# Optimization experiments

Measured on AMD Instinct MI355X. Metric: run time of the kernel, lower is better.

Reference implementation:

```python
import jax, jax.numpy as jnp
import numpy as np

ATTR_LEN = [2, 4, 4, 8]  # sums to 18 = MLP output dim; prod = 256 cases
USER_EMB_DIM = 256
B = 8192


def build_cases(attr_len):
    # Cartesian product of per-attribute one-hots -> [prod(attr_len), sum(attr_len)]
    out = np.eye(attr_len[0], dtype=np.float32)
    for n in attr_len[1:]:
        m = np.eye(n, dtype=np.float32)
        out = np.concatenate(
            [np.repeat(out, n, axis=0), np.tile(m, (out.shape[0], 1))], axis=1)
    return out


def setup_inputs() -> dict:
    key = jax.random.key(0)
    ks = jax.random.split(key, 8)
    d = USER_EMB_DIM
    x = jax.random.normal(ks[0], (B, d), dtype=jnp.float32)
    y = jax.random.uniform(ks[1], (B, 18), dtype=jnp.float32)
    # nn.Linear-style params (scaled normals)
    W1 = jax.random.normal(ks[2], (d, 50), dtype=jnp.float32) / np.sqrt(d)
    b1 = jnp.zeros((50,), dtype=jnp.float32)
    W2 = jax.random.normal(ks[3], (50, 32), dtype=jnp.float32) / np.sqrt(50.0)
    b2 = jnp.zeros((32,), dtype=jnp.float32)
    W3 = jax.random.normal(ks[4], (32, 18), dtype=jnp.float32) / np.sqrt(32.0)
    b3 = jnp.zeros((18,), dtype=jnp.float32)
    cases = jnp.asarray(build_cases(ATTR_LEN))  # [256, 18]
    return {"x": x, "y": y, "W1": W1, "b1": b1, "W2": W2, "b2": b2,
            "W3": W3, "b3": b3, "cases": cases}


def reference(x, y, W1, b1, W2, b2, W3, b3, cases):
    # MLP: user_emb_dim -> 50 -> 32 -> 18, sigmoid activations on hidden layers
    h = jax.nn.sigmoid(x @ W1 + b1)
    h = jax.nn.sigmoid(h @ W2 + b2)
    W_user = h @ W3 + b3                                  # [B, 18]
    # Partition function over all combinatorial label cases, fused into one
    # GEMM + logsumexp (original loops over cases with exp+accumulate).
    log_denom = jax.nn.logsumexp(W_user @ cases.T, axis=1)  # [B]
    # obj_i = exp(sum_j W_user[i].y[j]) / denom_i ; loss = -sum log obj
    S = jnp.sum(W_user @ y.T, axis=1)                     # [B] (via [B,B] mm, as original)
    loss = -jnp.sum(S - log_denom)
    # 'logit' in the original is W_user detached to numpy; return the array.
    return W_user, loss
```

## Files before the change

### kernel.cpp

```cpp
#include <hip/hip_runtime.h>

#define NB   8192
#define ND   256
#define NH1  50
#define NH2  32
#define NH3  18
#define RPB  16
#define NBLK (NB / RPB)
#define WSS  40


__device__ __forceinline__ float sigmoidf_fast(float v) {
    return 1.0f / (1.0f + __expf(-v));
}

template <int CTRL>
__device__ __forceinline__ float dpp_addf(float v) {
    return v + __int_as_float(__builtin_amdgcn_update_dpp(
        0, __float_as_int(v), CTRL, 0xF, 0xF, true));
}
__device__ __forceinline__ float sum16(float v) {
    v = dpp_addf<0xB1>(v);
    v = dpp_addf<0x4E>(v);
    v = dpp_addf<0x124>(v);
    v = dpp_addf<0x128>(v);
    return v;
}

__device__ __forceinline__ void gload_lds16(const float* g, float* l) {
    __builtin_amdgcn_global_load_lds(
        (const __attribute__((address_space(1))) unsigned int*)g,
        (__attribute__((address_space(3))) unsigned int*)l, 16, 0, 0);
}

__global__ __launch_bounds__(256) void fused_main(
    const float* __restrict__ x, const float* __restrict__ y,
    const float* __restrict__ W1, const float* __restrict__ b1,
    const float* __restrict__ W2, const float* __restrict__ b2,
    const float* __restrict__ W3, const float* __restrict__ b3,
    float* __restrict__ out, float* __restrict__ ws)
{
    __shared__ alignas(16) float w1l[ND * NH1];
    __shared__ alignas(16) float w2l[NH1 * NH2];
    __shared__ alignas(16) float w3l[NH2 * NH3];
    __shared__ alignas(16) float h2l[RPB][NH2 + 2];
    __shared__ alignas(16) float wul[RPB][NH3 + 1];

    const int t    = threadIdx.x;
    const int row  = t >> 4;
    const int ksl  = t & 15;
    const int lane = t & 63;
    const int wave = t >> 6;
    const int grow = blockIdx.x * RPB + row;

    const float* xrow = x + (size_t)grow * ND + 2 * ksl;
    float2 xv[8];
#pragma unroll
    for (int c = 0; c < 8; ++c)
        xv[c] = *reinterpret_cast<const float2*>(xrow + 32 * c);

#pragma unroll
    for (int i = 0; i < 13; ++i) {
        const int c = wave + 4 * i;
        if (c < 50)
            gload_lds16(W1 + c * 256 + lane * 4, w1l + c * 256);
    }
    for (int e = t; e < NH1 * NH2; e += 256) w2l[e] = W2[e];
    for (int e = t; e < NH2 * NH3; e += 256) w3l[e] = W3[e];
    __syncthreads();

    float h1[NH1];
#pragma unroll
    for (int j = 0; j < NH1; ++j) h1[j] = 0.0f;
#pragma unroll
    for (int c = 0; c < 8; ++c) {
        const int kA = 32 * c + 2 * ksl;
        const float* wA = &w1l[kA * NH1];
        const float* wB = wA + NH1;
        const float xa = xv[c].x, xb = xv[c].y;
#pragma unroll
        for (int jj = 0; jj < 25; ++jj) {
            const float2 a = *reinterpret_cast<const float2*>(wA + 2 * jj);
            const float2 b = *reinterpret_cast<const float2*>(wB + 2 * jj);
            h1[2 * jj]     = fmaf(xa, a.x, fmaf(xb, b.x, h1[2 * jj]));
            h1[2 * jj + 1] = fmaf(xa, a.y, fmaf(xb, b.y, h1[2 * jj + 1]));
        }
    }
#pragma unroll
    for (int j = 0; j < NH1; ++j)
        h1[j] = sigmoidf_fast(sum16(h1[j]) + b1[j]);

    {
        const float2 bb = *reinterpret_cast<const float2*>(b2 + 2 * ksl);
        float h2a = bb.x, h2b = bb.y;
#pragma unroll
        for (int j = 0; j < NH1; ++j) {
            const float2 w = *reinterpret_cast<const float2*>(&w2l[j * NH2 + 2 * ksl]);
            h2a = fmaf(h1[j], w.x, h2a);
            h2b = fmaf(h1[j], w.y, h2b);
        }
        h2a = sigmoidf_fast(h2a);
        h2b = sigmoidf_fast(h2b);
        *reinterpret_cast<float2*>(&h2l[row][2 * ksl]) = make_float2(h2a, h2b);
    }

    {
        float a0 = b3[ksl];
        float a1 = (ksl < 2) ? b3[16 + ksl] : 0.0f;
#pragma unroll
        for (int j = 0; j < NH2; ++j) {
            const float h = h2l[row][j];
            a0 = fmaf(h, w3l[j * NH3 + ksl], a0);
            if (ksl < 2) a1 = fmaf(h, w3l[j * NH3 + 16 + ksl], a1);
        }
        wul[row][ksl] = a0;
        out[(size_t)grow * NH3 + ksl] = a0;
        if (ksl < 2) {
            wul[row][16 + ksl] = a1;
            out[(size_t)grow * NH3 + 16 + ksl] = a1;
        }
    }
    __syncthreads();

    if (t < 64) {
        const bool act = t < RPB;
        float wv[NH3], yv[NH3];
        float ld = 0.0f;
        if (act) {
            const float* yrow = y + (size_t)(blockIdx.x * RPB + t) * NH3;
#pragma unroll
            for (int c = 0; c < NH3; ++c) {
                wv[c] = wul[t][c];
                yv[c] = yrow[c];
            }
            float m = fmaxf(wv[0], wv[1]);
            ld += m + __logf(__expf(wv[0] - m) + __expf(wv[1] - m));
            m = fmaxf(fmaxf(wv[2], wv[3]), fmaxf(wv[4], wv[5]));
            ld += m + __logf(__expf(wv[2] - m) + __expf(wv[3] - m) +
                             __expf(wv[4] - m) + __expf(wv[5] - m));
            m = fmaxf(fmaxf(wv[6], wv[7]), fmaxf(wv[8], wv[9]));
            ld += m + __logf(__expf(wv[6] - m) + __expf(wv[7] - m) +
                             __expf(wv[8] - m) + __expf(wv[9] - m));
            m = wv[10];
#pragma unroll
            for (int i = 11; i < NH3; ++i) m = fmaxf(m, wv[i]);
            float s = 0.0f;
#pragma unroll
            for (int i = 10; i < NH3; ++i) s += __expf(wv[i] - m);
            ld += m + __logf(s);
        } else {
#pragma unroll
            for (int c = 0; c < NH3; ++c) { wv[c] = 0.0f; yv[c] = 0.0f; }
        }

        ld = sum16(ld);
#pragma unroll
        for (int c = 0; c < NH3; ++c) {
            wv[c] = sum16(wv[c]);
            yv[c] = sum16(yv[c]);
        }
        if (t == 0) {
            float* slot = ws + (size_t)blockIdx.x * WSS;
#pragma unroll
            for (int c = 0; c < NH3; ++c) {
                slot[c]       = yv[c];
                slot[NH3 + c] = wv[c];
            }
            slot[36] = ld;
        }
    }
}

__global__ __launch_bounds__(256) void finalize_loss(
    const float* __restrict__ ws, float* __restrict__ out)
{
    __shared__ double part[4][37];
    const int t = threadIdx.x;
    const int w = t >> 6, l = t & 63;
    if (l < 37) {
        double a = 0.0;
        for (int b = w * (NBLK / 4); b < (w + 1) * (NBLK / 4); ++b)
            a += (double)ws[(size_t)b * WSS + l];
        part[w][l] = a;
    }
    __syncthreads();
    if (t == 0) {
        double tot[37];
#pragma unroll
        for (int c = 0; c < 37; ++c)
            tot[c] = part[0][c] + part[1][c] + part[2][c] + part[3][c];
        double s = 0.0;
#pragma unroll
        for (int c = 0; c < NH3; ++c)
            s += tot[NH3 + c] * tot[c];
        out[(size_t)NB * NH3] = (float)(-(s - tot[36]));
    }
}

extern "C" void kernel_launch(void* const* d_in, const int* in_sizes, int n_in,
                              void* d_out, int out_size, void* d_ws, size_t ws_size,
                              hipStream_t stream) {
    const float* x  = (const float*)d_in[0];
    const float* y  = (const float*)d_in[1];
    const float* W1 = (const float*)d_in[2];
    const float* b1 = (const float*)d_in[3];
    const float* W2 = (const float*)d_in[4];
    const float* b2 = (const float*)d_in[5];
    const float* W3 = (const float*)d_in[6];
    const float* b3 = (const float*)d_in[7];
    float* out = (float*)d_out;
    float* ws  = (float*)d_ws;

    fused_main<<<dim3(NBLK), dim3(256), 0, stream>>>(x, y, W1, b1, W2, b2, W3, b3, out, ws);
    finalize_loss<<<dim3(1), dim3(256), 0, stream>>>(ws, out);
}
```

Before: 94.73 us.

## Process two rows per thread with 128-thread blocks to reuse W1 LDS loads

Halves the block size to 128 threads and has each thread compute two batch rows (rs and rs+8). Each W1 value read from LDS now feeds FMAs for both rows, and the reads become float4 instead of paired float2. The goal is to cut LDS read traffic per FMA and the per-block cost of staging W1, W2 and W3. In exchange each thread holds twice as many accumulators (100 h1 values), which raises register pressure and may lower occupancy.

```diff
diff --git a/kernel.cpp b/kernel.cpp
--- a/kernel.cpp
+++ b/kernel.cpp
@@ -6,6 +6,7 @@
 #define NH2  32
 #define NH3  18
 #define RPB  16
+#define TPB  128
 #define NBLK (NB / RPB)
 #define WSS  40
 
@@ -33,7 +34,7 @@
         (__attribute__((address_space(3))) unsigned int*)l, 16, 0, 0);
 }
 
-__global__ __launch_bounds__(256) void fused_main(
+__global__ __launch_bounds__(TPB) void fused_main(
     const float* __restrict__ x, const float* __restrict__ y,
     const float* __restrict__ W1, const float* __restrict__ b1,
     const float* __restrict__ W2, const float* __restrict__ b2,
@@ -47,77 +48,106 @@
     __shared__ alignas(16) float wul[RPB][NH3 + 1];
 
     const int t    = threadIdx.x;
-    const int row  = t >> 4;
+    const int rs   = t >> 4;
     const int ksl  = t & 15;
     const int lane = t & 63;
     const int wave = t >> 6;
-    const int grow = blockIdx.x * RPB + row;
-
-    const float* xrow = x + (size_t)grow * ND + 2 * ksl;
-    float2 xv[8];
-#pragma unroll
-    for (int c = 0; c < 8; ++c)
-        xv[c] = *reinterpret_cast<const float2*>(xrow + 32 * c);
-
-#pragma unroll
-    for (int i = 0; i < 13; ++i) {
-        const int c = wave + 4 * i;
-        if (c < 50)
-            gload_lds16(W1 + c * 256 + lane * 4, w1l + c * 256);
-    }
-    for (int e = t; e < NH1 * NH2; e += 256) w2l[e] = W2[e];
-    for (int e = t; e < NH2 * NH3; e += 256) w3l[e] = W3[e];
+    const int g0   = blockIdx.x * RPB + rs;
+    const int g1   = g0 + 8;
+
+    const float* xr0 = x + (size_t)g0 * ND + 2 * ksl;
+    const float* xr1 = x + (size_t)g1 * ND + 2 * ksl;
+    float2 xv0[8], xv1[8];
+#pragma unroll
+    for (int c = 0; c < 8; ++c) {
+        xv0[c] = *reinterpret_cast<const float2*>(xr0 + 32 * c);
+        xv1[c] = *reinterpret_cast<const float2*>(xr1 + 32 * c);
+    }
+
+#pragma unroll
+    for (int i = 0; i < 25; ++i) {
+        const int c = wave + 2 * i;
+        gload_lds16(W1 + c * 256 + lane * 4, w1l + c * 256);
+    }
+    for (int e = t; e < NH1 * NH2; e += TPB) w2l[e] = W2[e];
+    for (int e = t; e < NH2 * NH3; e += TPB) w3l[e] = W3[e];
     __syncthreads();
 
-    float h1[NH1];
-#pragma unroll
-    for (int j = 0; j < NH1; ++j) h1[j] = 0.0f;
+    float h1a[NH1], h1b[NH1];
+#pragma unroll
+    for (int j = 0; j < NH1; ++j) { h1a[j] = 0.0f; h1b[j] = 0.0f; }
 #pragma unroll
     for (int c = 0; c < 8; ++c) {
         const int kA = 32 * c + 2 * ksl;
-        const float* wA = &w1l[kA * NH1];
-        const float* wB = wA + NH1;
-        const float xa = xv[c].x, xb = xv[c].y;
-#pragma unroll
-        for (int jj = 0; jj < 25; ++jj) {
-            const float2 a = *reinterpret_cast<const float2*>(wA + 2 * jj);
-            const float2 b = *reinterpret_cast<const float2*>(wB + 2 * jj);
-            h1[2 * jj]     = fmaf(xa, a.x, fmaf(xb, b.x, h1[2 * jj]));
-            h1[2 * jj + 1] = fmaf(xa, a.y, fmaf(xb, b.y, h1[2 * jj + 1]));
-        }
-    }
-#pragma unroll
-    for (int j = 0; j < NH1; ++j)
-        h1[j] = sigmoidf_fast(sum16(h1[j]) + b1[j]);
+        const float* wp = &w1l[kA * NH1];
+        const float xa0 = xv0[c].x, xb0 = xv0[c].y;
+        const float xa1 = xv1[c].x, xb1 = xv1[c].y;
+#pragma unroll
+        for (int q = 0; q < 25; ++q) {
+            const float4 w = *reinterpret_cast<const float4*>(wp + 4 * q);
+            const float we[4] = {w.x, w.y, w.z, w.w};
+#pragma unroll
+            for (int s = 0; s < 4; ++s) {
+                const int e = 4 * q + s;
+                if (e < NH1) {
+                    h1a[e] = fmaf(xa0, we[s], h1a[e]);
+                    h1b[e] = fmaf(xa1, we[s], h1b[e]);
+                } else {
+                    h1a[e - NH1] = fmaf(xb0, we[s], h1a[e - NH1]);
+                    h1b[e - NH1] = fmaf(xb1, we[s], h1b[e - NH1]);
+                }
+            }
+        }
+    }
+#pragma unroll
+    for (int j = 0; j < NH1; ++j) {
+        h1a[j] = sigmoidf_fast(sum16(h1a[j]) + b1[j]);
+        h1b[j] = sigmoidf_fast(sum16(h1b[j]) + b1[j]);
+    }
 
     {
         const float2 bb = *reinterpret_cast<const float2*>(b2 + 2 * ksl);
-        float h2a = bb.x, h2b = bb.y;
+        float aa0 = bb.x, aa1 = bb.y, ba0 = bb.x, ba1 = bb.y;
 #pragma unroll
         for (int j = 0; j < NH1; ++j) {
             const float2 w = *reinterpret_cast<const float2*>(&w2l[j * NH2 + 2 * ksl]);
-            h2a = fmaf(h1[j], w.x, h2a);
-            h2b = fmaf(h1[j], w.y, h2b);
-        }
-        h2a = sigmoidf_fast(h2a);
-        h2b = sigmoidf_fast(h2b);
-        *reinterpret_cast<float2*>(&h2l[row][2 * ksl]) = make_float2(h2a, h2b);
+            aa0 = fmaf(h1a[j], w.x, aa0);
+            aa1 = fmaf(h1a[j], w.y, aa1);
+            ba0 = fmaf(h1b[j], w.x, ba0);
+            ba1 = fmaf(h1b[j], w.y, ba1);
+        }
+        *reinterpret_cast<float2*>(&h2l[rs][2 * ksl]) =
+            make_float2(sigmoidf_fast(aa0), sigmoidf_fast(aa1));
+        *reinterpret_cast<float2*>(&h2l[rs + 8][2 * ksl]) =
+            make_float2(sigmoidf_fast(ba0), sigmoidf_fast(ba1));
     }
 
     {
-        float a0 = b3[ksl];
-        float a1 = (ksl < 2) ? b3[16 + ksl] : 0.0f;
+        float a0A = b3[ksl], a0B = b3[ksl];
+        float a1A = (ksl < 2) ? b3[16 + ksl] : 0.0f;
+        float a1B = a1A;
 #pragma unroll
         for (int j = 0; j < NH2; ++j) {
-            const float h = h2l[row][j];
-            a0 = fmaf(h, w3l[j * NH3 + ksl], a0);
-            if (ksl < 2) a1 = fmaf(h, w3l[j * NH3 + 16 + ksl], a1);
-        }
-        wul[row][ksl] = a0;
-        out[(size_t)grow * NH3 + ksl] = a0;
+            const float hA = h2l[rs][j];
+            const float hB = h2l[rs + 8][j];
+            const float w3v = w3l[j * NH3 + ksl];
+            a0A = fmaf(hA, w3v, a0A);
+            a0B = fmaf(hB, w3v, a0B);
+            if (ksl < 2) {
+                const float w3x = w3l[j * NH3 + 16 + ksl];
+                a1A = fmaf(hA, w3x, a1A);
+                a1B = fmaf(hB, w3x, a1B);
+            }
+        }
+        wul[rs][ksl] = a0A;
+        wul[rs + 8][ksl] = a0B;
+        out[(size_t)g0 * NH3 + ksl] = a0A;
+        out[(size_t)g1 * NH3 + ksl] = a0B;
         if (ksl < 2) {
-            wul[row][16 + ksl] = a1;
-            out[(size_t)grow * NH3 + 16 + ksl] = a1;
+            wul[rs][16 + ksl] = a1A;
+            wul[rs + 8][16 + ksl] = a1B;
+            out[(size_t)g0 * NH3 + 16 + ksl] = a1A;
+            out[(size_t)g1 * NH3 + 16 + ksl] = a1B;
         }
     }
     __syncthreads();
@@ -211,6 +241,6 @@
     float* out = (float*)d_out;
     float* ws  = (float*)d_ws;
 
-    fused_main<<<dim3(NBLK), dim3(256), 0, stream>>>(x, y, W1, b1, W2, b2, W3, b3, out, ws);
+    fused_main<<<dim3(NBLK), dim3(TPB), 0, stream>>>(x, y, W1, b1, W2, b2, W3, b3, out, ws);
     finalize_loss<<<dim3(1), dim3(256), 0, stream>>>(ws, out);
 }
```

Result: slower. 101.0 us (+6.7%).

## Keep W1 in registers and stage x tile in LDS for layer one

Applied to the files above, without the earlier changes.

Layer one no longer loads the whole 50 KB W1 into LDS in each block. Each thread now holds a 64-element slice of W1 in registers, read straight from global memory, and the block's 16 x rows go into LDS through direct global-to-LDS loads. Partial sums are reduced with DPP, and h1 passes through LDS to layer two. This is meant to cut LDS footprint and per-block staging traffic so more blocks fit per CU, at the cost of higher register pressure and uncoalesced W1 reads from global. The final reduction also gets four independent accumulators to expose more ILP.

```diff
diff --git a/kernel.cpp b/kernel.cpp
--- a/kernel.cpp
+++ b/kernel.cpp
@@ -6,6 +6,7 @@
 #define NH2  32
 #define NH3  18
 #define RPB  16
+#define TPB  256
 #define NBLK (NB / RPB)
 #define WSS  40
 
@@ -33,75 +34,98 @@
         (__attribute__((address_space(3))) unsigned int*)l, 16, 0, 0);
 }
 
-__global__ __launch_bounds__(256) void fused_main(
+__global__ __launch_bounds__(TPB) void fused_main(
     const float* __restrict__ x, const float* __restrict__ y,
     const float* __restrict__ W1, const float* __restrict__ b1,
     const float* __restrict__ W2, const float* __restrict__ b2,
     const float* __restrict__ W3, const float* __restrict__ b3,
     float* __restrict__ out, float* __restrict__ ws)
 {
-    __shared__ alignas(16) float w1l[ND * NH1];
+    __shared__ alignas(16) float xl[RPB * ND];
+    __shared__ alignas(16) float h1l[RPB][52];
     __shared__ alignas(16) float w2l[NH1 * NH2];
     __shared__ alignas(16) float w3l[NH2 * NH3];
     __shared__ alignas(16) float h2l[RPB][NH2 + 2];
     __shared__ alignas(16) float wul[RPB][NH3 + 1];
 
     const int t    = threadIdx.x;
-    const int row  = t >> 4;
     const int ksl  = t & 15;
+    const int jsl  = t >> 4;
     const int lane = t & 63;
     const int wave = t >> 6;
+
+    const float* xblk = x + (size_t)blockIdx.x * RPB * ND;
+#pragma unroll
+    for (int i = 0; i < 4; ++i) {
+        const int r = wave + 4 * i;
+        gload_lds16(xblk + r * ND + lane * 4, xl + r * ND);
+    }
+
+    float w1r[4][4][4];
+    float b1r[4];
+#pragma unroll
+    for (int s = 0; s < 3; ++s) b1r[s] = b1[jsl + 16 * s];
+    b1r[3] = (jsl < 2) ? b1[jsl + 48] : 0.0f;
+#pragma unroll
+    for (int q = 0; q < 4; ++q) {
+#pragma unroll
+        for (int i = 0; i < 4; ++i) {
+            const int k = 64 * q + 4 * ksl + i;
+            const float* wk = W1 + k * NH1;
+#pragma unroll
+            for (int s = 0; s < 3; ++s) w1r[q][i][s] = wk[jsl + 16 * s];
+            w1r[q][i][3] = (jsl < 2) ? wk[jsl + 48] : 0.0f;
+        }
+    }
+
+    for (int e = t; e < NH1 * NH2; e += TPB) w2l[e] = W2[e];
+    for (int e = t; e < NH2 * NH3; e += TPB) w3l[e] = W3[e];
+    __syncthreads();
+
+#pragma unroll 4
+    for (int r = 0; r < RPB; ++r) {
+        float4 xq[4];
+#pragma unroll
+        for (int q = 0; q < 4; ++q)
+            xq[q] = *reinterpret_cast<const float4*>(&xl[r * ND + 64 * q + 4 * ksl]);
+        float acc[4] = {0.0f, 0.0f, 0.0f, 0.0f};
+#pragma unroll
+        for (int q = 0; q < 4; ++q) {
+            const float xe[4] = {xq[q].x, xq[q].y, xq[q].z, xq[q].w};
+#pragma unroll
+            for (int i = 0; i < 4; ++i) {
+#pragma unroll
+                for (int s = 0; s < 4; ++s)
+                    acc[s] = fmaf(xe[i], w1r[q][i][s], acc[s]);
+            }
+        }
+#pragma unroll
+        for (int s = 0; s < 4; ++s) acc[s] = sum16(acc[s]);
+        if (ksl == r) {
+#pragma unroll
+            for (int s = 0; s < 3; ++s)
+                h1l[r][jsl + 16 * s] = sigmoidf_fast(acc[s] + b1r[s]);
+            if (jsl < 2)
+                h1l[r][jsl + 48] = sigmoidf_fast(acc[3] + b1r[3]);
+        }
+    }
+    __syncthreads();
+
+    const int row  = jsl;
     const int grow = blockIdx.x * RPB + row;
-
-    const float* xrow = x + (size_t)grow * ND + 2 * ksl;
-    float2 xv[8];
-#pragma unroll
-    for (int c = 0; c < 8; ++c)
-        xv[c] = *reinterpret_cast<const float2*>(xrow + 32 * c);
-
-#pragma unroll
-    for (int i = 0; i < 13; ++i) {
-        const int c = wave + 4 * i;
-        if (c < 50)
-            gload_lds16(W1 + c * 256 + lane * 4, w1l + c * 256);
-    }
-    for (int e = t; e < NH1 * NH2; e += 256) w2l[e] = W2[e];
-    for (int e = t; e < NH2 * NH3; e += 256) w3l[e] = W3[e];
-    __syncthreads();
-
-    float h1[NH1];
-#pragma unroll
-    for (int j = 0; j < NH1; ++j) h1[j] = 0.0f;
-#pragma unroll
-    for (int c = 0; c < 8; ++c) {
-        const int kA = 32 * c + 2 * ksl;
-        const float* wA = &w1l[kA * NH1];
-        const float* wB = wA + NH1;
-        const float xa = xv[c].x, xb = xv[c].y;
-#pragma unroll
-        for (int jj = 0; jj < 25; ++jj) {
-            const float2 a = *reinterpret_cast<const float2*>(wA + 2 * jj);
-            const float2 b = *reinterpret_cast<const float2*>(wB + 2 * jj);
-            h1[2 * jj]     = fmaf(xa, a.x, fmaf(xb, b.x, h1[2 * jj]));
-            h1[2 * jj + 1] = fmaf(xa, a.y, fmaf(xb, b.y, h1[2 * jj + 1]));
-        }
-    }
-#pragma unroll
-    for (int j = 0; j < NH1; ++j)
-        h1[j] = sigmoidf_fast(sum16(h1[j]) + b1[j]);
-
     {
         const float2 bb = *reinterpret_cast<const float2*>(b2 + 2 * ksl);
         float h2a = bb.x, h2b = bb.y;
 #pragma unroll
-        for (int j = 0; j < NH1; ++j) {
-            const float2 w = *reinterpret_cast<const float2*>(&w2l[j * NH2 + 2 * ksl]);
-            h2a = fmaf(h1[j], w.x, h2a);
-            h2b = fmaf(h1[j], w.y, h2b);
-        }
-        h2a = sigmoidf_fast(h2a);
-        h2b = sigmoidf_fast(h2b);
-        *reinterpret_cast<float2*>(&h2l[row][2 * ksl]) = make_float2(h2a, h2b);
+        for (int jj = 0; jj < 25; ++jj) {
+            const float2 hh = *reinterpret_cast<const float2*>(&h1l[row][2 * jj]);
+            const float2 wA = *reinterpret_cast<const float2*>(&w2l[(2 * jj)     * NH2 + 2 * ksl]);
+            const float2 wB = *reinterpret_cast<const float2*>(&w2l[(2 * jj + 1) * NH2 + 2 * ksl]);
+            h2a = fmaf(hh.x, wA.x, fmaf(hh.y, wB.x, h2a));
+            h2b = fmaf(hh.x, wA.y, fmaf(hh.y, wB.y, h2b));
+        }
+        *reinterpret_cast<float2*>(&h2l[row][2 * ksl]) =
+            make_float2(sigmoidf_fast(h2a), sigmoidf_fast(h2b));
     }
 
     {
@@ -178,10 +202,15 @@
     const int t = threadIdx.x;
     const int w = t >> 6, l = t & 63;
     if (l < 37) {
-        double a = 0.0;
-        for (int b = w * (NBLK / 4); b < (w + 1) * (NBLK / 4); ++b)
-            a += (double)ws[(size_t)b * WSS + l];
-        part[w][l] = a;
+        double a0 = 0.0, a1 = 0.0, a2 = 0.0, a3 = 0.0;
+        const int base = w * (NBLK / 4);
+        for (int b = 0; b < NBLK / 4; b += 4) {
+            a0 += (double)ws[(size_t)(base + b    ) * WSS + l];
+            a1 += (double)ws[(size_t)(base + b + 1) * WSS + l];
+            a2 += (double)ws[(size_t)(base + b + 2) * WSS + l];
+            a3 += (double)ws[(size_t)(base + b + 3) * WSS + l];
+        }
+        part[w][l] = (a0 + a1) + (a2 + a3);
     }
     __syncthreads();
     if (t == 0) {
@@ -211,6 +240,6 @@
     float* out = (float*)d_out;
     float* ws  = (float*)d_ws;
 
-    fused_main<<<dim3(NBLK), dim3(256), 0, stream>>>(x, y, W1, b1, W2, b2, W3, b3, out, ws);
+    fused_main<<<dim3(NBLK), dim3(TPB), 0, stream>>>(x, y, W1, b1, W2, b2, W3, b3, out, ws);
     finalize_loss<<<dim3(1), dim3(256), 0, stream>>>(ws, out);
 }
```

Result: slower. 104.6 us (+10.4%).
